# Optimization experiments

Hardware: AMD Instinct MI355X
Metric: run time of the kernel (lower is better)

The kernel has to match this reference:

```python
import jax, jax.numpy as jnp
import numpy as np
from jax import lax

NUM_CLASSES = 91
C_FEAT = 2048
HF = WF = 16          # backbone feature map size (512px image / stride 32)
STRIDE = 32           # anchor stride, as in source generate_base_anchors
N_ANCHOR_TYPES = 9
NMS_THR = 0.5
K_ROIS = 100          # fixed proposal count after NMS (padded, jit-safe)
SPATIAL_SCALE = 1.0 / 16.0
POOL = 7
SR = 2                # sampling ratio (source uses adaptive -1; fixed here)


def conv2d(x, w, b, pad):
    y = lax.conv_general_dilated(x, w, (1, 1), pad,
                                 dimension_numbers=('NCHW', 'OIHW', 'NCHW'))
    return y + b[None, :, None, None]


def setup_inputs():
    key = jax.random.key(0)
    ks = jax.random.split(key, 16)
    f32 = jnp.float32
    def w(k, shape, s=0.01):
        return jax.random.normal(k, shape, f32) * s
    z = lambda n: jnp.zeros((n,), f32)
    D = C_FEAT * POOL * POOL  # 100352
    return dict(
        x=jax.random.normal(ks[0], (1, C_FEAT, HF, WF), f32),
        rpn_w=w(ks[1], (512, C_FEAT, 3, 3)), rpn_b=z(512),
        cls_w=w(ks[2], (18, 512, 1, 1)), cls_b=z(18),
        bbox_w=w(ks[3], (36, 512, 1, 1)), bbox_b=z(36),
        fc1c_w=w(ks[4], (D, 4096)), fc1c_b=z(4096),
        fc2c_w=w(ks[5], (4096, NUM_CLASSES)), fc2c_b=z(NUM_CLASSES),
        fc1b_w=w(ks[6], (D, 4096)), fc1b_b=z(4096),
        fc2b_w=w(ks[7], (4096, 4)), fc2b_b=z(4),
        m1_w=w(ks[8], (256, C_FEAT, 3, 3)), m1_b=z(256),
        mt_w=w(ks[9], (256, 256, 2, 2)), mt_b=z(256),  # ConvT weight [C_in,C_out,kh,kw]
        m2_w=w(ks[10], (1, 256, 1, 1)), m2_b=z(1),
    )


def _anchors(hf, wf):
    scales = jnp.array([8.0, 16.0, 32.0])
    ratios = jnp.array([0.5, 1.0, 2.0])
    ws = (scales[:, None] * jnp.sqrt(ratios)[None, :]).reshape(-1)  # scale-major, 9
    hs = (scales[:, None] / jnp.sqrt(ratios)[None, :]).reshape(-1)
    base = jnp.stack([-ws / 2, -hs / 2, ws / 2, hs / 2], axis=1)    # [9,4]
    sy, sx = jnp.meshgrid(jnp.arange(hf) * STRIDE, jnp.arange(wf) * STRIDE, indexing='ij')
    shifts = jnp.stack([sx, sy, sx, sy], -1).reshape(-1, 4).astype(jnp.float32)  # [HW,4]
    return (base[:, None, :] + shifts[None, :, :]).reshape(-1, 4)   # [9*HW,4] anchor-type major


def _decode(a, d):
    wa = a[:, 2] - a[:, 0]
    ha = a[:, 3] - a[:, 1]
    cx = a[:, 0] + 0.5 * wa
    cy = a[:, 1] + 0.5 * ha
    px = cx + d[:, 0] * wa
    py = cy + d[:, 1] * ha
    pw = jnp.exp(d[:, 2]) * wa
    ph = jnp.exp(d[:, 3]) * ha
    return jnp.stack([px - 0.5 * pw, py - 0.5 * ph, px + 0.5 * pw, py + 0.5 * ph], 1)


def _nms_topk(boxes, scores, thr, k):
    n = boxes.shape[0]
    order = jnp.argsort(-scores)
    b = boxes[order]
    s = scores[order]
    area = (b[:, 2] - b[:, 0]) * (b[:, 3] - b[:, 1])
    xx1 = jnp.maximum(b[:, None, 0], b[None, :, 0])
    yy1 = jnp.maximum(b[:, None, 1], b[None, :, 1])
    xx2 = jnp.minimum(b[:, None, 2], b[None, :, 2])
    yy2 = jnp.minimum(b[:, None, 3], b[None, :, 3])
    inter = jnp.clip(xx2 - xx1, 0) * jnp.clip(yy2 - yy1, 0)
    iou = inter / (area[:, None] + area[None, :] - inter + 1e-9)
    j = jnp.arange(n)
    def body(i, keep):
        sup = keep[i] & (iou[i] > thr) & (j > i)
        return keep & ~sup
    keep = lax.fori_loop(0, n, body, jnp.ones((n,), bool))
    masked = jnp.where(keep, s, -jnp.inf)
    vals, pos = lax.top_k(masked, k)
    valid = jnp.isfinite(vals)
    fb = jnp.where(valid[:, None], b[pos], 0.0)
    fs = jnp.where(valid, vals, 0.0)
    return fb, fs


def _roi_align(feat, boxes):
    # feat: [C,H,W]; boxes: [K,4] in image coords
    C, H, W = feat.shape
    r = boxes * SPATIAL_SCALE
    S = POOL * SR  # 14 sample points per side
    t = (jnp.arange(S, dtype=feat.dtype) + 0.5) / S
    gx = jnp.clip(r[:, 0:1] + t[None, :] * (r[:, 2:3] - r[:, 0:1]), 0.0, W - 1.0)
    gy = jnp.clip(r[:, 1:2] + t[None, :] * (r[:, 3:4] - r[:, 1:2]), 0.0, H - 1.0)
    x0 = jnp.floor(gx); y0 = jnp.floor(gy)
    lx = gx - x0; ly = gy - y0
    x0i = x0.astype(jnp.int32); y0i = y0.astype(jnp.int32)
    x1i = jnp.minimum(x0i + 1, W - 1); y1i = jnp.minimum(y0i + 1, H - 1)
    flat = feat.reshape(C, H * W)
    def g(yi, xi):  # yi:[K,S] row coords, xi:[K,S] col coords -> [C,K,S,S]
        idx = yi[:, :, None] * W + xi[:, None, :]
        return flat[:, idx]
    lyb = ly[:, :, None]; lxb = lx[:, None, :]
    v = ((1 - lyb) * (1 - lxb) * g(y0i, x0i)
         + (1 - lyb) * lxb * g(y0i, x1i)
         + lyb * (1 - lxb) * g(y1i, x0i)
         + lyb * lxb * g(y1i, x1i))  # [C,K,S,S]
    v = v.reshape(C, -1, POOL, SR, POOL, SR).mean(axis=(3, 5))
    return v.transpose(1, 0, 2, 3)  # [K,C,7,7]


def reference(x, rpn_w, rpn_b, cls_w, cls_b, bbox_w, bbox_b,
              fc1c_w, fc1c_b, fc2c_w, fc2c_b,
              fc1b_w, fc1b_b, fc2b_w, fc2b_b,
              m1_w, m1_b, mt_w, mt_b, m2_w, m2_b):
    p1 = [(1, 1), (1, 1)]; p0 = [(0, 0), (0, 0)]
    f = jax.nn.relu(conv2d(x, rpn_w, rpn_b, p1))      # [1,512,H,W]
    obj = conv2d(f, cls_w, cls_b, p0)                 # [1,18,H,W]
    deltas = conv2d(f, bbox_w, bbox_b, p0)            # [1,36,H,W]
    hf, wf = f.shape[2], f.shape[3]
    hw = hf * wf
    # softmax over the 2 objectness classes (view(B,2,-1) layout)
    scores = jax.nn.softmax(obj.reshape(2, N_ANCHOR_TYPES, hw), axis=0)[1].reshape(-1)
    d = deltas.reshape(N_ANCHOR_TYPES, 4, hw).transpose(0, 2, 1).reshape(-1, 4)
    anchors = _anchors(hf, wf)
    boxes = _decode(anchors, d)
    fb, fs = _nms_topk(boxes, scores, NMS_THR, K_ROIS)
    rois = _roi_align(x[0], fb)                       # [K,2048,7,7]
    flat = rois.reshape(K_ROIS, -1)
    cls_out = jax.nn.relu(flat @ fc1c_w + fc1c_b) @ fc2c_w + fc2c_b
    box_out = jax.nn.relu(flat @ fc1b_w + fc1b_b) @ fc2b_w + fc2b_b
    m = jax.nn.relu(conv2d(rois, m1_w, m1_b, p1))     # [K,256,7,7]
    # ConvTranspose2d(k=2,s=2): non-overlapping, each pixel expands to a 2x2 block
    up = jnp.einsum('nchw,coij->nohiwj', m, mt_w).reshape(K_ROIS, 256, 2 * POOL, 2 * POOL)
    m = jax.nn.relu(up + mt_b[None, :, None, None])
    masks = conv2d(m, m2_w, m2_b, p0)                 # [K,1,14,14]
    return cls_out, box_out, masks
```

## Files before the change

### kernel.cpp

```cpp
#include <hip/hip_runtime.h>

#define DEVFN __device__ __forceinline__

typedef unsigned short ushort_t;
typedef unsigned int uint32;
typedef __attribute__((ext_vector_type(8))) short bf16x8;
typedef __attribute__((ext_vector_type(4))) float f32x4;

DEVFN ushort_t f2bf(float x) {
    uint32 b = __float_as_uint(x);
    uint32 r = (b + 0x7FFFu + ((b >> 16) & 1u)) >> 16;
    return (ushort_t)r;
}
DEVFN float bf2f(ushort_t u) { return __uint_as_float(((uint32)u) << 16); }

__global__ __launch_bounds__(256) void k_prep(const float* __restrict__ m1_w,
                                              const float* __restrict__ mt_w,
                                              const float* __restrict__ x,
                                              ushort_t* __restrict__ wAf,
                                              ushort_t* __restrict__ wA2f,
                                              float* __restrict__ xt) {
    const int bid = blockIdx.x, tid = threadIdx.x;
    if (bid < 256) {
        const int p = bid * 4 + (tid >> 6);
        const int lane = tid & 63, l15 = lane & 15, lg = lane >> 4;
        const int cot = p >> 6, cis = p & 63;
        const int co = cot * 16 + l15, k0 = cis * 32 + lg * 8;
        const float* src = m1_w + ((size_t)co * 2048 + k0) * 9;
        float v[72];
#pragma unroll
        for (int i = 0; i < 72; ++i) v[i] = src[i];
#pragma unroll
        for (int tap = 0; tap < 9; ++tap) {
            ushort_t* dst = wAf + ((size_t)((tap * 16 + cot) * 64 + cis) * 512) + lane * 8;
            ushort_t t8[8];
#pragma unroll
            for (int j = 0; j < 8; ++j) t8[j] = f2bf(v[j * 9 + tap]);
            uint4 u;
            u.x = (uint32)t8[0] | ((uint32)t8[1] << 16);
            u.y = (uint32)t8[2] | ((uint32)t8[3] << 16);
            u.z = (uint32)t8[4] | ((uint32)t8[5] << 16);
            u.w = (uint32)t8[6] | ((uint32)t8[7] << 16);
            *(uint4*)dst = u;
        }
    } else if (bid < 1280) {
        int idx = (bid - 256) * 256 + tid;
        int j = idx & 7, lane = (idx >> 3) & 63, cis = (idx >> 9) & 7, cot = idx >> 12;
        int row = cot * 16 + (lane & 15);
        int c = cis * 32 + (lane >> 4) * 8 + j;
        int o = row >> 2, ij = row & 3;
        wA2f[idx] = f2bf(mt_w[((size_t)c * 256 + o) * 4 + ij]);
    } else {
        int pos = bid - 1280;
        for (int i = 0; i < 8; ++i) {
            int c = tid + i * 256;
            xt[(size_t)pos * 2048 + c] = x[(size_t)c * 256 + pos];
        }
    }
}

__global__ __launch_bounds__(256) void k_rpn(const float* __restrict__ x,
                                             const float* __restrict__ rpn_w,
                                             float* __restrict__ fpart) {
    __shared__ float xs[8][18][18];
    const int coP = blockIdx.x, ks = blockIdx.y, tid = threadIdx.x;
    const int ty = tid >> 4, tx = tid & 15;
    const int co0 = coP * 4;
    for (int i = tid; i < 8 * 18 * 18; i += 256) ((float*)xs)[i] = 0.f;
    float acc[4] = {0.f, 0.f, 0.f, 0.f};
    for (int ch = 0; ch < 32; ++ch) {
        const int cib = ks * 256 + ch * 8;
        __syncthreads();
#pragma unroll
        for (int cc = 0; cc < 8; ++cc) xs[cc][ty + 1][tx + 1] = x[(size_t)(cib + cc) * 256 + tid];
        __syncthreads();
#pragma unroll
        for (int cc = 0; cc < 8; ++cc) {
            const int ci = cib + cc;
            float v[9];
#pragma unroll
            for (int t = 0; t < 9; ++t) v[t] = xs[cc][ty + t / 3][tx + t % 3];
            const float* wb = rpn_w + ((size_t)co0 * 2048 + ci) * 9;
#pragma unroll
            for (int o = 0; o < 4; ++o) {
                const float* w = wb + (size_t)o * 2048 * 9;
#pragma unroll
                for (int t = 0; t < 9; ++t) acc[o] = fmaf(v[t], w[t], acc[o]);
            }
        }
    }
#pragma unroll
    for (int o = 0; o < 4; ++o) fpart[((size_t)ks * 512 + co0 + o) * 256 + tid] = acc[o];
}

__global__ void k_rpn_reduce(const float* __restrict__ fpart, const float* __restrict__ rpn_b,
                             float* __restrict__ f) {
    const int i = blockIdx.x * 256 + threadIdx.x;
    float s = 0.f;
#pragma unroll
    for (int p = 0; p < 8; ++p) s += fpart[(size_t)p * 131072 + i];
    f[i] = fmaxf(s + rpn_b[i >> 8], 0.f);
}

__global__ void k_head(const float* __restrict__ f, const float* __restrict__ cls_w,
                       const float* __restrict__ cls_b, const float* __restrict__ bbox_w,
                       const float* __restrict__ bbox_b, float* __restrict__ scores,
                       float* __restrict__ boxes) {
    const int a = blockIdx.x, pos = threadIdx.x;
    float o0 = 0, o1 = 0, d0 = 0, d1 = 0, d2 = 0, d3 = 0;
    const float* c0 = cls_w + (size_t)a * 512;
    const float* c1 = cls_w + (size_t)(9 + a) * 512;
    const float* b0p = bbox_w + (size_t)(4 * a) * 512;
    const float* b1p = b0p + 512;
    const float* b2p = b0p + 1024;
    const float* b3p = b0p + 1536;
    for (int ci = 0; ci < 512; ++ci) {
        float fv = f[(size_t)ci * 256 + pos];
        o0 = fmaf(c0[ci], fv, o0);
        o1 = fmaf(c1[ci], fv, o1);
        d0 = fmaf(b0p[ci], fv, d0);
        d1 = fmaf(b1p[ci], fv, d1);
        d2 = fmaf(b2p[ci], fv, d2);
        d3 = fmaf(b3p[ci], fv, d3);
    }
    o0 += cls_b[a]; o1 += cls_b[9 + a];
    d0 += bbox_b[4 * a + 0]; d1 += bbox_b[4 * a + 1];
    d2 += bbox_b[4 * a + 2]; d3 += bbox_b[4 * a + 3];
    float mx = fmaxf(o0, o1);
    float e0 = expf(o0 - mx), e1 = expf(o1 - mx);
    float sc = e1 / (e0 + e1);
    int si = a / 3, ri = a % 3;
    float scale = (si == 0) ? 8.f : ((si == 1) ? 16.f : 32.f);
    float ratio = (ri == 0) ? 0.5f : ((ri == 1) ? 1.f : 2.f);
    float sq = sqrtf(ratio);
    float hw2 = (scale * sq) * 0.5f;
    float hh2 = (scale / sq) * 0.5f;
    int py = pos >> 4, px = pos & 15;
    float sx = (float)(px * 32), sy = (float)(py * 32);
    float a0 = sx - hw2, a1 = sy - hh2, a2 = sx + hw2, a3 = sy + hh2;
    float wa = a2 - a0, ha = a3 - a1;
    float cx = a0 + 0.5f * wa, cy = a1 + 0.5f * ha;
    float pxc = cx + d0 * wa, pyc = cy + d1 * ha;
    float pw = expf(d2) * wa, ph = expf(d3) * ha;
    int idx = a * 256 + pos;
    scores[idx] = sc;
    boxes[idx * 4 + 0] = pxc - 0.5f * pw;
    boxes[idx * 4 + 1] = pyc - 0.5f * ph;
    boxes[idx * 4 + 2] = pxc + 0.5f * pw;
    boxes[idx * 4 + 3] = pyc + 0.5f * ph;
}

__global__ void k_sort(const float* __restrict__ scores, const float* __restrict__ boxes,
                       float* __restrict__ ssort, float* __restrict__ bsort) {
    const int i = blockIdx.x * 256 + threadIdx.x;
    const float si = scores[i];
    int rank = 0;
    for (int j = 0; j < 2304; ++j) {
        float sj = scores[j];
        rank += (sj > si) || (sj == si && j < i);
    }
    ssort[rank] = si;
    float4 bb = *(const float4*)(boxes + (size_t)i * 4);
    *(float4*)(bsort + (size_t)rank * 4) = bb;
}

__global__ void k_adj(const float* __restrict__ bsort, unsigned long long* __restrict__ adj) {
    const int i = blockIdx.x, lane = threadIdx.x;
    const float4 bi = *(const float4*)(bsort + (size_t)i * 4);
    const float ai = (bi.z - bi.x) * (bi.w - bi.y);
    for (int w = 0; w < 36; ++w) {
        int j = w * 64 + lane;
        bool sup = false;
        if (j < 2304 && j > i) {
            float4 bj = *(const float4*)(bsort + (size_t)j * 4);
            float aj = (bj.z - bj.x) * (bj.w - bj.y);
            float xx1 = fmaxf(bi.x, bj.x), yy1 = fmaxf(bi.y, bj.y);
            float xx2 = fminf(bi.z, bj.z), yy2 = fminf(bi.w, bj.w);
            float inter = fmaxf(xx2 - xx1, 0.f) * fmaxf(yy2 - yy1, 0.f);
            float iou = inter / (ai + aj - inter + 1e-9f);
            sup = iou > 0.5f;
        }
        unsigned long long m = __ballot(sup);
        if (lane == 0) adj[(size_t)i * 36 + w] = m;
    }
}

__global__ void k_nms(const unsigned long long* __restrict__ adj, const float* __restrict__ bsort,
                      float* __restrict__ fb) {
    const int lane = threadIdx.x;
    unsigned long long r = (lane < 36) ? 0ULL : ~0ULL;
    int cnt = 0;
    for (int it = 0; it < 128; ++it) {
        unsigned long long inv = ~r;
        int local = inv ? (__ffsll((unsigned long long)inv) - 1) : 64;
        int cand = (local < 64) ? lane * 64 + local : (1 << 30);
#pragma unroll
        for (int d = 32; d; d >>= 1) cand = min(cand, __shfl_xor(cand, d));
        if (cand >= 2304) break;
        if (lane == 0) *(float4*)(fb + (size_t)cnt * 4) = *(const float4*)(bsort + (size_t)cand * 4);
        ++cnt;
        if (cnt == 100) break;
        unsigned long long a = (lane < 36) ? adj[(size_t)cand * 36 + lane] : 0ULL;
        r |= a;
        if (lane == (cand >> 6)) r |= 1ULL << (cand & 63);
    }
    for (int s2 = lane; s2 < 100; s2 += 64)
        if (s2 >= cnt) {
            float4 z = {0.f, 0.f, 0.f, 0.f};
            *(float4*)(fb + (size_t)s2 * 4) = z;
        }
}

__global__ __launch_bounds__(256) void k_roi(const float* __restrict__ xt,
                                             const float* __restrict__ fb,
                                             ushort_t* __restrict__ flatA,
                                             ushort_t* __restrict__ flatT) {
    __shared__ int sxi0[14], sxi1[14], syi0[14], syi1[14];
    __shared__ float slx[14], sly[14];
    const int cg = blockIdx.x, n = blockIdx.y, tid = threadIdx.x;
    const float r0 = fb[n * 4 + 0] * 0.0625f, r1 = fb[n * 4 + 1] * 0.0625f;
    const float r2 = fb[n * 4 + 2] * 0.0625f, r3 = fb[n * 4 + 3] * 0.0625f;
    if (tid < 14) {
        float tt = ((float)tid + 0.5f) * (1.0f / 14.0f);
        float gx = r0 + tt * (r2 - r0);
        gx = fminf(fmaxf(gx, 0.f), 15.f);
        float x0f = floorf(gx);
        int x0 = (int)x0f;
        sxi0[tid] = x0; sxi1[tid] = min(x0 + 1, 15); slx[tid] = gx - x0f;
        float gy = r1 + tt * (r3 - r1);
        gy = fminf(fmaxf(gy, 0.f), 15.f);
        float y0f = floorf(gy);
        int y0 = (int)y0f;
        syi0[tid] = y0; syi1[tid] = min(y0 + 1, 15); sly[tid] = gy - y0f;
    }
    __syncthreads();
    const int c = cg * 256 + tid;
    for (int py = 0; py < 7; ++py) {
        for (int px = 0; px < 7; ++px) {
            float accv = 0.f;
#pragma unroll
            for (int a2 = 0; a2 < 2; ++a2) {
                int sy = py * 2 + a2;
                int y0 = syi0[sy], y1 = syi1[sy];
                float ly = sly[sy];
#pragma unroll
                for (int b2 = 0; b2 < 2; ++b2) {
                    int sx = px * 2 + b2;
                    int x0 = sxi0[sx], x1 = sxi1[sx];
                    float lx = slx[sx];
                    float v00 = xt[(size_t)(y0 * 16 + x0) * 2048 + c];
                    float v01 = xt[(size_t)(y0 * 16 + x1) * 2048 + c];
                    float v10 = xt[(size_t)(y1 * 16 + x0) * 2048 + c];
                    float v11 = xt[(size_t)(y1 * 16 + x1) * 2048 + c];
                    accv += (1.f - ly) * (1.f - lx) * v00 + (1.f - ly) * lx * v01 +
                            ly * (1.f - lx) * v10 + ly * lx * v11;
                }
            }
            ushort_t bv = f2bf(accv * 0.25f);
            int pos = py * 7 + px;
            flatT[((size_t)n * 49 + pos) * 2048 + c] = bv;
            int k = c * 49 + pos;
            flatA[((size_t)(k >> 5) * 112 + n) * 32 + (k & 31)] = bv;
        }
    }
}

__global__ __launch_bounds__(256) void k_big(const ushort_t* __restrict__ flatA,
                                             const ushort_t* __restrict__ flatT,
                                             const float* __restrict__ Wc,
                                             const float* __restrict__ Wb,
                                             float* __restrict__ part,
                                             const ushort_t* __restrict__ wAf,
                                             const float* __restrict__ m1_b,
                                             ushort_t* __restrict__ m1outT) {
    const int bid = blockIdx.x, tid = threadIdx.x;
    const int wave = tid >> 6, lane = tid & 63, l15 = lane & 15, lg = lane >> 4;
    const f32x4 zz = {0.f, 0.f, 0.f, 0.f};
    if (bid < 77) {
        const int nb = bid;
        int nn[4], ppy[4], ppx[4], colv[4];
#pragma unroll
        for (int nt = 0; nt < 4; ++nt) {
            int col = nb * 64 + nt * 16 + l15;
            colv[nt] = col;
            int n = col / 49;
            int pos = col - n * 49;
            nn[nt] = n;
            ppy[nt] = pos / 7;
            ppx[nt] = pos - (pos / 7) * 7;
        }
        f32x4 acc[4][4];
#pragma unroll
        for (int a = 0; a < 4; ++a)
#pragma unroll
            for (int b = 0; b < 4; ++b) acc[a][b] = zz;
        bf16x8 zfrag;
#pragma unroll
        for (int j = 0; j < 8; ++j) zfrag[j] = 0;
        for (int tap = 0; tap < 9; ++tap) {
            const int ty = tap / 3 - 1, tx = tap % 3 - 1;
            int val[4];
            size_t bofs[4];
#pragma unroll
            for (int nt = 0; nt < 4; ++nt) {
                int iy = ppy[nt] + ty, ix = ppx[nt] + tx;
                val[nt] = (iy >= 0 && iy < 7 && ix >= 0 && ix < 7);
                bofs[nt] = ((size_t)nn[nt] * 49 + iy * 7 + ix) * 2048;
            }
            for (int cis = 0; cis < 64; ++cis) {
                const int kq = cis * 32 + lg * 8;
                bf16x8 a[4];
#pragma unroll
                for (int mt = 0; mt < 4; ++mt)
                    a[mt] = *(const bf16x8*)(wAf +
                            ((size_t)((tap * 16 + wave * 4 + mt) * 64 + cis) * 64 + lane) * 8);
                bf16x8 b[4];
#pragma unroll
                for (int nt = 0; nt < 4; ++nt)
                    b[nt] = val[nt] ? *(const bf16x8*)(flatT + bofs[nt] + kq) : zfrag;
#pragma unroll
                for (int nt = 0; nt < 4; ++nt)
#pragma unroll
                    for (int mt = 0; mt < 4; ++mt)
                        acc[mt][nt] = __builtin_amdgcn_mfma_f32_16x16x32_bf16(a[mt], b[nt], acc[mt][nt], 0, 0, 0);
            }
        }
#pragma unroll
        for (int mt = 0; mt < 4; ++mt)
#pragma unroll
            for (int nt = 0; nt < 4; ++nt) {
                int co0 = wave * 64 + mt * 16 + lg * 4;
                ushort_t v[4];
#pragma unroll
                for (int r = 0; r < 4; ++r)
                    v[r] = f2bf(fmaxf(acc[mt][nt][r] + m1_b[co0 + r], 0.f));
                uint2 u;
                u.x = (uint32)v[0] | ((uint32)v[1] << 16);
                u.y = (uint32)v[2] | ((uint32)v[3] << 16);
                *(uint2*)(m1outT + (size_t)colv[nt] * 256 + co0) = u;
            }
        return;
    }
    const int b = bid - 77;
    const int x = b & 7, i = b >> 3;
    const int nb = i & 31;
    const int g = x + 8 * (i >> 5);
    const int kc = g >> 1, br = g & 1;
    const float* W = br ? Wb : Wc;
    const int ncol0 = nb * 128 + wave * 32;
    const size_t wstep = (size_t)32 * 4096;
    const float* wp = W + ((size_t)kc * 196 * 32 + lg * 8) * 4096 + ncol0 + l15;
    const ushort_t* ap = flatA + ((size_t)kc * 196 * 112 + l15) * 32 + lg * 8;
    float wc[16], wn[16];
#pragma unroll
    for (int j = 0; j < 8; ++j) {
        wc[j] = wp[(size_t)j * 4096];
        wc[8 + j] = wp[(size_t)j * 4096 + 16];
    }
    f32x4 acc0[7], acc1[7];
#pragma unroll
    for (int t = 0; t < 7; ++t) { acc0[t] = zz; acc1[t] = zz; }
    for (int s = 0; s < 196; s += 2) {
        const float* wp1 = wp + wstep;
#pragma unroll
        for (int j = 0; j < 8; ++j) {
            wn[j] = wp1[(size_t)j * 4096];
            wn[8 + j] = wp1[(size_t)j * 4096 + 16];
        }
        bf16x8 af[7];
#pragma unroll
        for (int t = 0; t < 7; ++t) af[t] = *(const bf16x8*)(ap + (size_t)t * 512);
        bf16x8 b0, b1;
#pragma unroll
        for (int j = 0; j < 8; ++j) {
            b0[j] = (short)f2bf(wc[j]);
            b1[j] = (short)f2bf(wc[8 + j]);
        }
#pragma unroll
        for (int t = 0; t < 7; ++t) {
            acc0[t] = __builtin_amdgcn_mfma_f32_16x16x32_bf16(af[t], b0, acc0[t], 0, 0, 0);
            acc1[t] = __builtin_amdgcn_mfma_f32_16x16x32_bf16(af[t], b1, acc1[t], 0, 0, 0);
        }
        const float* wp2 = (s + 2 < 196) ? wp + 2 * wstep : wp;
#pragma unroll
        for (int j = 0; j < 8; ++j) {
            wc[j] = wp2[(size_t)j * 4096];
            wc[8 + j] = wp2[(size_t)j * 4096 + 16];
        }
        bf16x8 af2[7];
#pragma unroll
        for (int t = 0; t < 7; ++t) af2[t] = *(const bf16x8*)(ap + 3584 + (size_t)t * 512);
#pragma unroll
        for (int j = 0; j < 8; ++j) {
            b0[j] = (short)f2bf(wn[j]);
            b1[j] = (short)f2bf(wn[8 + j]);
        }
#pragma unroll
        for (int t = 0; t < 7; ++t) {
            acc0[t] = __builtin_amdgcn_mfma_f32_16x16x32_bf16(af2[t], b0, acc0[t], 0, 0, 0);
            acc1[t] = __builtin_amdgcn_mfma_f32_16x16x32_bf16(af2[t], b1, acc1[t], 0, 0, 0);
        }
        wp += 2 * wstep;
        ap += 2 * 3584;
    }
    float* pb = part + (size_t)(br * 16 + kc) * 112 * 4096;
#pragma unroll
    for (int t = 0; t < 7; ++t)
#pragma unroll
        for (int r = 0; r < 4; ++r) {
            int m = t * 16 + lg * 4 + r;
            pb[(size_t)m * 4096 + ncol0 + l15] = acc0[t][r];
            pb[(size_t)m * 4096 + ncol0 + 16 + l15] = acc1[t][r];
        }
}

__global__ __launch_bounds__(256) void k_fc2(const float* __restrict__ part,
                                             const float* __restrict__ fc1c_b,
                                             const float* __restrict__ fc1b_b,
                                             const float* __restrict__ Wc,
                                             const float* __restrict__ bc,
                                             const float* __restrict__ Wb,
                                             const float* __restrict__ bb,
                                             float* __restrict__ out) {
    __shared__ float h_s[2][4096];
    const int m = blockIdx.x, tid = threadIdx.x;
    for (int i = tid; i < 8192; i += 256) {
        int br = i >> 12, col = i & 4095;
        float s = br ? fc1b_b[col] : fc1c_b[col];
#pragma unroll
        for (int p = 0; p < 16; ++p) s += part[((size_t)(br * 16 + p) * 112 + m) * 4096 + col];
        h_s[br][col] = fmaxf(s, 0.f);
    }
    __syncthreads();
    if (tid < 91) {
        float acc = bc[tid];
        for (int k = 0; k < 4096; ++k) acc = fmaf(h_s[0][k], Wc[(size_t)k * 91 + tid], acc);
        out[m * 91 + tid] = acc;
    } else if (tid >= 96 && tid < 100) {
        int col = tid - 96;
        float acc = bb[col];
        for (int k = 0; k < 4096; ++k) acc = fmaf(h_s[1][k], Wb[(size_t)k * 4 + col], acc);
        out[9100 + m * 4 + col] = acc;
    }
}

__global__ __launch_bounds__(256) void k_up(const ushort_t* __restrict__ m1outT,
                                            const ushort_t* __restrict__ wA2f,
                                            ushort_t* __restrict__ upT) {
    const int nb = blockIdx.x, cq = blockIdx.y, tid = threadIdx.x;
    const int wave = tid >> 6, lane = tid & 63, l15 = lane & 15, lg = lane >> 4;
    int colv[4];
#pragma unroll
    for (int nt = 0; nt < 4; ++nt) colv[nt] = nb * 64 + nt * 16 + l15;
    f32x4 acc[4][4];
    const f32x4 zz = {0.f, 0.f, 0.f, 0.f};
#pragma unroll
    for (int a = 0; a < 4; ++a)
#pragma unroll
        for (int b = 0; b < 4; ++b) acc[a][b] = zz;
    for (int cis = 0; cis < 8; ++cis) {
        const int kq = cis * 32 + lg * 8;
        bf16x8 a[4];
#pragma unroll
        for (int mt = 0; mt < 4; ++mt)
            a[mt] = *(const bf16x8*)(wA2f +
                    ((size_t)((cq * 16 + wave * 4 + mt) * 8 + cis) * 64 + lane) * 8);
        bf16x8 b[4];
#pragma unroll
        for (int nt = 0; nt < 4; ++nt)
            b[nt] = *(const bf16x8*)(m1outT + (size_t)colv[nt] * 256 + kq);
#pragma unroll
        for (int nt = 0; nt < 4; ++nt)
#pragma unroll
            for (int mt = 0; mt < 4; ++mt)
                acc[mt][nt] = __builtin_amdgcn_mfma_f32_16x16x32_bf16(a[mt], b[nt], acc[mt][nt], 0, 0, 0);
    }
#pragma unroll
    for (int mt = 0; mt < 4; ++mt)
#pragma unroll
        for (int nt = 0; nt < 4; ++nt) {
            int rb = (cq * 16 + wave * 4 + mt) * 16 + lg * 4;
            ushort_t v[4];
#pragma unroll
            for (int r = 0; r < 4; ++r) v[r] = f2bf(acc[mt][nt][r]);
            uint2 u;
            u.x = (uint32)v[0] | ((uint32)v[1] << 16);
            u.y = (uint32)v[2] | ((uint32)v[3] << 16);
            *(uint2*)(upT + (size_t)colv[nt] * 1024 + rb) = u;
        }
}

__global__ void k_mask(const ushort_t* __restrict__ upT, const float* __restrict__ mt_b,
                       const float* __restrict__ m2_w, const float* __restrict__ m2_b,
                       float* __restrict__ out) {
    const int n = blockIdx.x, t = threadIdx.x;
    if (t >= 196) return;
    const int ys = t / 14, xs = t % 14;
    const int ro = (ys & 1) * 2 + (xs & 1);
    const int col = n * 49 + (ys >> 1) * 7 + (xs >> 1);
    float acc = m2_b[0];
    for (int o = 0; o < 256; ++o) {
        float v = bf2f(upT[(size_t)col * 1024 + o * 4 + ro]) + mt_b[o];
        v = fmaxf(v, 0.f);
        acc = fmaf(m2_w[o], v, acc);
    }
    out[9500 + n * 196 + t] = acc;
}

extern "C" void kernel_launch(void* const* d_in, const int* in_sizes, int n_in,
                              void* d_out, int out_size, void* d_ws, size_t ws_size,
                              hipStream_t stream) {
    const float* x      = (const float*)d_in[0];
    const float* rpn_w  = (const float*)d_in[1];
    const float* rpn_b  = (const float*)d_in[2];
    const float* cls_w  = (const float*)d_in[3];
    const float* cls_b  = (const float*)d_in[4];
    const float* bbox_w = (const float*)d_in[5];
    const float* bbox_b = (const float*)d_in[6];
    const float* fc1c_w = (const float*)d_in[7];
    const float* fc1c_b = (const float*)d_in[8];
    const float* fc2c_w = (const float*)d_in[9];
    const float* fc2c_b = (const float*)d_in[10];
    const float* fc1b_w = (const float*)d_in[11];
    const float* fc1b_b = (const float*)d_in[12];
    const float* fc2b_w = (const float*)d_in[13];
    const float* fc2b_b = (const float*)d_in[14];
    const float* m1_w   = (const float*)d_in[15];
    const float* m1_b   = (const float*)d_in[16];
    const float* mt_w   = (const float*)d_in[17];
    const float* mt_b   = (const float*)d_in[18];
    const float* m2_w   = (const float*)d_in[19];
    const float* m2_b   = (const float*)d_in[20];
    float* out = (float*)d_out;

    char* ws = (char*)d_ws;
    size_t off = 0;
    auto take = [&](size_t nbytes) -> char* {
        char* p = ws + off;
        off += (nbytes + 255) & ~(size_t)255;
        return p;
    };
    float* xt      = (float*)take(2097152);
    float* fpart   = (float*)take(4194304);
    float* f       = (float*)take(524288);
    float* scores  = (float*)take(9216);
    float* boxes   = (float*)take(36864);
    float* ssort   = (float*)take(9216);
    float* bsort   = (float*)take(36864);
    unsigned long long* adj = (unsigned long long*)take(663552);
    float* fb      = (float*)take(1600);
    ushort_t* flatA = (ushort_t*)take(22478848);
    ushort_t* flatT = (ushort_t*)take(20471808);
    float* part1   = (float*)take(58720256);
    ushort_t* wAf  = (ushort_t*)take(9437184);
    ushort_t* m1outT = (ushort_t*)take(2523136);
    ushort_t* wA2f = (ushort_t*)take(524288);
    ushort_t* upT  = (ushort_t*)part1;

    k_prep<<<1536, 256, 0, stream>>>(m1_w, mt_w, x, wAf, wA2f, xt);
    k_rpn<<<dim3(128, 8), 256, 0, stream>>>(x, rpn_w, fpart);
    k_rpn_reduce<<<512, 256, 0, stream>>>(fpart, rpn_b, f);
    k_head<<<9, 256, 0, stream>>>(f, cls_w, cls_b, bbox_w, bbox_b, scores, boxes);
    k_sort<<<9, 256, 0, stream>>>(scores, boxes, ssort, bsort);
    k_adj<<<2304, 64, 0, stream>>>(bsort, adj);
    k_nms<<<1, 64, 0, stream>>>(adj, bsort, fb);
    k_roi<<<dim3(8, 100), 256, 0, stream>>>(xt, fb, flatA, flatT);
    k_big<<<1101, 256, 0, stream>>>(flatA, flatT, fc1c_w, fc1b_w, part1, wAf, m1_b, m1outT);
    k_fc2<<<100, 256, 0, stream>>>(part1, fc1c_b, fc1b_b, fc2c_w, fc2c_b, fc2b_w, fc2b_b, out);
    k_up<<<dim3(77, 4), 256, 0, stream>>>(m1outT, wA2f, upT);
    k_mask<<<100, 256, 0, stream>>>(upT, mt_b, m2_w, m2_b, out);
}
```

Baseline: 1.686 ms.

## Split fc1 GEMM finer over K and N, use packed bf16 convert, unroll reductions

The fc1 part of k_big now splits K into 28 chunks instead of 16 and N into 64-column blocks, with each wave handling 16 columns, so the grid grows from 1101 to 3661 blocks. The aim is more parallelism for streaming the large fp32 weight matrices across the CUs. Weight conversion to bf16 now uses the packed v_cvt_pk_bf16_f32 instruction instead of manual rounding. k_fc2 and k_mask get four independent accumulators to break serial FMA chains. The trade-off is a larger partial-sum buffer and more partials that k_fc2 must reduce, plus fewer MFMAs per weight load.

Result: slower. 2.183 ms (+29.5%).

```diff
diff --git a/kernel.cpp b/kernel.cpp
--- a/kernel.cpp
+++ b/kernel.cpp
@@ -13,6 +13,8 @@
     return (ushort_t)r;
 }
 DEVFN float bf2f(ushort_t u) { return __uint_as_float(((uint32)u) << 16); }
+
+union BWU { uint32 u[4]; bf16x8 v8; };
 
 __global__ __launch_bounds__(256) void k_prep(const float* __restrict__ m1_w,
                                               const float* __restrict__ mt_w,
@@ -341,76 +343,60 @@
             }
         return;
     }
-    const int b = bid - 77;
-    const int x = b & 7, i = b >> 3;
-    const int nb = i & 31;
-    const int g = x + 8 * (i >> 5);
+    const int h = bid - 77;
+    const int x = bid & 7;
+    const int q = h >> 3;
+    const int nb = q & 63;
+    const int g = x + 8 * (q >> 6);
     const int kc = g >> 1, br = g & 1;
     const float* W = br ? Wb : Wc;
-    const int ncol0 = nb * 128 + wave * 32;
+    const int ncol0 = nb * 64 + wave * 16;
     const size_t wstep = (size_t)32 * 4096;
-    const float* wp = W + ((size_t)kc * 196 * 32 + lg * 8) * 4096 + ncol0 + l15;
-    const ushort_t* ap = flatA + ((size_t)kc * 196 * 112 + l15) * 32 + lg * 8;
-    float wc[16], wn[16];
-#pragma unroll
-    for (int j = 0; j < 8; ++j) {
-        wc[j] = wp[(size_t)j * 4096];
-        wc[8 + j] = wp[(size_t)j * 4096 + 16];
-    }
-    f32x4 acc0[7], acc1[7];
-#pragma unroll
-    for (int t = 0; t < 7; ++t) { acc0[t] = zz; acc1[t] = zz; }
-    for (int s = 0; s < 196; s += 2) {
+    const float* wp = W + ((size_t)(kc * 112) * 32 + lg * 8) * 4096 + ncol0 + l15;
+    const ushort_t* ap = flatA + ((size_t)(kc * 112) * 112 + l15) * 32 + lg * 8;
+    float wc[8], wn[8];
+#pragma unroll
+    for (int j = 0; j < 8; ++j) wc[j] = wp[(size_t)j * 4096];
+    f32x4 acc0[7];
+#pragma unroll
+    for (int t = 0; t < 7; ++t) acc0[t] = zz;
+    for (int s = 0; s < 112; s += 2) {
         const float* wp1 = wp + wstep;
 #pragma unroll
-        for (int j = 0; j < 8; ++j) {
-            wn[j] = wp1[(size_t)j * 4096];
-            wn[8 + j] = wp1[(size_t)j * 4096 + 16];
-        }
+        for (int j = 0; j < 8; ++j) wn[j] = wp1[(size_t)j * 4096];
         bf16x8 af[7];
 #pragma unroll
         for (int t = 0; t < 7; ++t) af[t] = *(const bf16x8*)(ap + (size_t)t * 512);
-        bf16x8 b0, b1;
-#pragma unroll
-        for (int j = 0; j < 8; ++j) {
-            b0[j] = (short)f2bf(wc[j]);
-            b1[j] = (short)f2bf(wc[8 + j]);
-        }
-#pragma unroll
-        for (int t = 0; t < 7; ++t) {
-            acc0[t] = __builtin_amdgcn_mfma_f32_16x16x32_bf16(af[t], b0, acc0[t], 0, 0, 0);
-            acc1[t] = __builtin_amdgcn_mfma_f32_16x16x32_bf16(af[t], b1, acc1[t], 0, 0, 0);
-        }
-        const float* wp2 = (s + 2 < 196) ? wp + 2 * wstep : wp;
-#pragma unroll
-        for (int j = 0; j < 8; ++j) {
-            wc[j] = wp2[(size_t)j * 4096];
-            wc[8 + j] = wp2[(size_t)j * 4096 + 16];
-        }
+        BWU b0u;
+#pragma unroll
+        for (int j = 0; j < 4; ++j)
+            asm("v_cvt_pk_bf16_f32 %0, %1, %2" : "=v"(b0u.u[j]) : "v"(wc[2 * j]), "v"(wc[2 * j + 1]));
+#pragma unroll
+        for (int t = 0; t < 7; ++t)
+            acc0[t] = __builtin_amdgcn_mfma_f32_16x16x32_bf16(af[t], b0u.v8, acc0[t], 0, 0, 0);
+        const float* wp2 = (s + 2 < 112) ? wp + 2 * wstep : wp;
+#pragma unroll
+        for (int j = 0; j < 8; ++j) wc[j] = wp2[(size_t)j * 4096];
         bf16x8 af2[7];
 #pragma unroll
         for (int t = 0; t < 7; ++t) af2[t] = *(const bf16x8*)(ap + 3584 + (size_t)t * 512);
-#pragma unroll
-        for (int j = 0; j < 8; ++j) {
-            b0[j] = (short)f2bf(wn[j]);
-            b1[j] = (short)f2bf(wn[8 + j]);
-        }
-#pragma unroll
-        for (int t = 0; t < 7; ++t) {
-            acc0[t] = __builtin_amdgcn_mfma_f32_16x16x32_bf16(af2[t], b0, acc0[t], 0, 0, 0);
-            acc1[t] = __builtin_amdgcn_mfma_f32_16x16x32_bf16(af2[t], b1, acc1[t], 0, 0, 0);
-        }
+        BWU b1u;
+#pragma unroll
+        for (int j = 0; j < 4; ++j)
+            asm("v_cvt_pk_bf16_f32 %0, %1, %2" : "=v"(b1u.u[j]) : "v"(wn[2 * j]), "v"(wn[2 * j + 1]));
+#pragma unroll
+        for (int t = 0; t < 7; ++t)
+            acc0[t] = __builtin_amdgcn_mfma_f32_16x16x32_bf16(af2[t], b1u.v8, acc0[t], 0, 0, 0);
         wp += 2 * wstep;
         ap += 2 * 3584;
     }
-    float* pb = part + (size_t)(br * 16 + kc) * 112 * 4096;
+    float* pb = part + (size_t)(br * 28 + kc) * 112 * 4096;
 #pragma unroll
     for (int t = 0; t < 7; ++t)
 #pragma unroll
         for (int r = 0; r < 4; ++r) {
             int m = t * 16 + lg * 4 + r;
             pb[(size_t)m * 4096 + ncol0 + l15] = acc0[t][r];
-            pb[(size_t)m * 4096 + ncol0 + 16 + l15] = acc1[t][r];
         }
 }
 
@@ -428,19 +414,33 @@
         int br = i >> 12, col = i & 4095;
         float s = br ? fc1b_b[col] : fc1c_b[col];
 #pragma unroll
-        for (int p = 0; p < 16; ++p) s += part[((size_t)(br * 16 + p) * 112 + m) * 4096 + col];
+        for (int p = 0; p < 28; ++p) s += part[((size_t)(br * 28 + p) * 112 + m) * 4096 + col];
         h_s[br][col] = fmaxf(s, 0.f);
     }
     __syncthreads();
     if (tid < 91) {
-        float acc = bc[tid];
-        for (int k = 0; k < 4096; ++k) acc = fmaf(h_s[0][k], Wc[(size_t)k * 91 + tid], acc);
-        out[m * 91 + tid] = acc;
+        const float* wcol = Wc + tid;
+        float a0 = bc[tid], a1 = 0.f, a2 = 0.f, a3 = 0.f;
+#pragma unroll 4
+        for (int k = 0; k < 4096; k += 4) {
+            a0 = fmaf(h_s[0][k],     wcol[(size_t)k * 91], a0);
+            a1 = fmaf(h_s[0][k + 1], wcol[(size_t)(k + 1) * 91], a1);
+            a2 = fmaf(h_s[0][k + 2], wcol[(size_t)(k + 2) * 91], a2);
+            a3 = fmaf(h_s[0][k + 3], wcol[(size_t)(k + 3) * 91], a3);
+        }
+        out[m * 91 + tid] = (a0 + a1) + (a2 + a3);
     } else if (tid >= 96 && tid < 100) {
         int col = tid - 96;
-        float acc = bb[col];
-        for (int k = 0; k < 4096; ++k) acc = fmaf(h_s[1][k], Wb[(size_t)k * 4 + col], acc);
-        out[9100 + m * 4 + col] = acc;
+        const float* wcol = Wb + col;
+        float a0 = bb[col], a1 = 0.f, a2 = 0.f, a3 = 0.f;
+#pragma unroll 4
+        for (int k = 0; k < 4096; k += 4) {
+            a0 = fmaf(h_s[1][k],     wcol[(size_t)k * 4], a0);
+            a1 = fmaf(h_s[1][k + 1], wcol[(size_t)(k + 1) * 4], a1);
+            a2 = fmaf(h_s[1][k + 2], wcol[(size_t)(k + 2) * 4], a2);
+            a3 = fmaf(h_s[1][k + 3], wcol[(size_t)(k + 3) * 4], a3);
+        }
+        out[9100 + m * 4 + col] = (a0 + a1) + (a2 + a3);
     }
 }
 
@@ -498,13 +498,16 @@
     const int ys = t / 14, xs = t % 14;
     const int ro = (ys & 1) * 2 + (xs & 1);
     const int col = n * 49 + (ys >> 1) * 7 + (xs >> 1);
-    float acc = m2_b[0];
-    for (int o = 0; o < 256; ++o) {
-        float v = bf2f(upT[(size_t)col * 1024 + o * 4 + ro]) + mt_b[o];
-        v = fmaxf(v, 0.f);
-        acc = fmaf(m2_w[o], v, acc);
-    }
-    out[9500 + n * 196 + t] = acc;
+    const ushort_t* up0 = upT + (size_t)col * 1024 + ro;
+    float a0 = m2_b[0], a1 = 0.f, a2 = 0.f, a3 = 0.f;
+#pragma unroll 4
+    for (int o = 0; o < 256; o += 4) {
+        a0 = fmaf(m2_w[o],     fmaxf(bf2f(up0[(o) * 4]) + mt_b[o], 0.f), a0);
+        a1 = fmaf(m2_w[o + 1], fmaxf(bf2f(up0[(o + 1) * 4]) + mt_b[o + 1], 0.f), a1);
+        a2 = fmaf(m2_w[o + 2], fmaxf(bf2f(up0[(o + 2) * 4]) + mt_b[o + 2], 0.f), a2);
+        a3 = fmaf(m2_w[o + 3], fmaxf(bf2f(up0[(o + 3) * 4]) + mt_b[o + 3], 0.f), a3);
+    }
+    out[9500 + n * 196 + t] = (a0 + a1) + (a2 + a3);
 }
 
 extern "C" void kernel_launch(void* const* d_in, const int* in_sizes, int n_in,
@@ -551,7 +554,7 @@
     float* fb      = (float*)take(1600);
     ushort_t* flatA = (ushort_t*)take(22478848);
     ushort_t* flatT = (ushort_t*)take(20471808);
-    float* part1   = (float*)take(58720256);
+    float* part1   = (float*)take(102760448);
     ushort_t* wAf  = (ushort_t*)take(9437184);
     ushort_t* m1outT = (ushort_t*)take(2523136);
     ushort_t* wA2f = (ushort_t*)take(524288);
@@ -565,7 +568,7 @@
     k_adj<<<2304, 64, 0, stream>>>(bsort, adj);
     k_nms<<<1, 64, 0, stream>>>(adj, bsort, fb);
     k_roi<<<dim3(8, 100), 256, 0, stream>>>(xt, fb, flatA, flatT);
-    k_big<<<1101, 256, 0, stream>>>(flatA, flatT, fc1c_w, fc1b_w, part1, wAf, m1_b, m1outT);
+    k_big<<<3661, 256, 0, stream>>>(flatA, flatT, fc1c_w, fc1b_w, part1, wAf, m1_b, m1outT);
     k_fc2<<<100, 256, 0, stream>>>(part1, fc1c_b, fc1b_b, fc2c_w, fc2c_b, fc2b_w, fc2b_b, out);
     k_up<<<dim3(77, 4), 256, 0, stream>>>(m1outT, wA2f, upT);
     k_mask<<<100, 256, 0, stream>>>(upT, mt_b, m2_w, m2_b, out);
```
